# Kernel tuning notes

Measured on AMD Instinct MI355X. Metric: run time of the kernel, lower is better.

Reference implementation:

```python
import jax, jax.numpy as jnp
import numpy as np

N = 100000          # nodes
E = 300000          # edges
F_IN = 128          # num_features
H = 256             # hidden_size
C = 1               # num_classes
G = 2048            # number of graphs in batch
EPS = 1e-5


def setup_inputs() -> dict:
    key = jax.random.key(0)
    ks = jax.random.split(key, 16)
    x = jax.random.normal(ks[0], (N, F_IN), dtype=jnp.float32)
    edge_index = jax.random.randint(ks[1], (2, E), 0, N, dtype=jnp.int64)
    batch = jnp.sort(jax.random.randint(ks[2], (N,), 0, G, dtype=jnp.int64))

    def glorot(k, shape):
        lim = np.sqrt(6.0 / (shape[0] + shape[1]))
        return jax.random.uniform(k, shape, jnp.float32, -lim, lim)

    return {
        "x": x, "edge_index": edge_index, "batch": batch,
        "W1": glorot(ks[3], (F_IN, H)), "b1": jnp.zeros((H,), jnp.float32),
        "W2": glorot(ks[4], (H, H)),    "b2": jnp.zeros((H,), jnp.float32),
        "W3": glorot(ks[5], (H, H)),    "b3": jnp.zeros((H,), jnp.float32),
        "g1": jnp.ones((H,), jnp.float32),  "be1": jnp.zeros((H,), jnp.float32),
        "g2": jnp.ones((H,), jnp.float32),  "be2": jnp.zeros((H,), jnp.float32),
        "g3": jnp.ones((H,), jnp.float32),  "be3": jnp.zeros((H,), jnp.float32),
        "LW1": glorot(ks[6], (H, H)),   "Lb1": jnp.zeros((H,), jnp.float32),
        "LW2": glorot(ks[7], (H, C)),   "Lb2": jnp.zeros((C,), jnp.float32),
    }


def _gcn_conv(x, W, b, src, dst, dinv):
    xw = x @ W                                       # [N, H]
    coeff = (dinv[src] * dinv[dst])[:, None]          # [E, 1]
    msg = xw[src] * coeff                             # gather + scale, [E, H]
    agg = jax.ops.segment_sum(msg, dst, num_segments=x.shape[0])  # scatter-add
    agg = agg + xw * (dinv * dinv)[:, None]           # self-loop term
    return agg + b


def _bn_relu(h, g, be):
    # BatchNorm1d in training mode: batch stats over nodes (biased variance)
    m = h.mean(axis=0)
    v = h.var(axis=0)
    return jax.nn.relu((h - m) * jax.lax.rsqrt(v + EPS) * g + be)


def reference(x, edge_index, batch, W1, b1, W2, b2, W3, b3,
              g1, be1, g2, be2, g3, be3, LW1, Lb1, LW2, Lb2):
    src = edge_index[0]
    dst = edge_index[1]
    # degree with self-loops (computed at destination, as in PyG)
    deg = jax.ops.segment_sum(jnp.ones((E,), jnp.float32), dst, num_segments=N) + 1.0
    dinv = jax.lax.rsqrt(deg)

    h = _bn_relu(_gcn_conv(x, W1, b1, src, dst, dinv), g1, be1)
    h = _bn_relu(_gcn_conv(h, W2, b2, src, dst, dinv), g2, be2)
    h = _bn_relu(_gcn_conv(h, W3, b3, src, dst, dinv), g3, be3)

    # global_add_pool: sum node features per graph
    pooled = jax.ops.segment_sum(h, batch, num_segments=G)   # [G, H]

    out = jax.nn.relu(pooled @ LW1 + Lb1)
    out = out @ LW2 + Lb2                                    # [G, 1]
    return jnp.squeeze(out, axis=1)                          # [G]
```

## Files before the change

### kernel.cpp

```cpp
#include <hip/hip_runtime.h>


typedef __attribute__((ext_vector_type(8))) short bf16x8;
typedef __attribute__((ext_vector_type(4))) float f32x4;

__device__ inline float bf2f(unsigned short u) {
    union { unsigned int i; float f; } v; v.i = ((unsigned int)u) << 16; return v.f;
}
__device__ inline unsigned short f2bf(float f) {
    unsigned int x = __float_as_uint(f);
    unsigned int r = (x + 0x7FFFu + ((x >> 16) & 1u)) >> 16;
    return (unsigned short)r;
}

__device__ inline float4 ld4u(const unsigned short* p) {
    ushort4 u = *(const ushort4*)p;
    return make_float4(bf2f(u.x), bf2f(u.y), bf2f(u.z), bf2f(u.w));
}
__device__ inline void st4u(unsigned short* p, float4 v) {
    ushort4 u; u.x = f2bf(v.x); u.y = f2bf(v.y); u.z = f2bf(v.z); u.w = f2bf(v.w);
    *(ushort4*)p = u;
}

__global__ void count_deg_i(const int* __restrict__ dst, int* __restrict__ deg, int E) {
    int i = blockIdx.x * blockDim.x + threadIdx.x;
    int stride = gridDim.x * blockDim.x;
    for (; i < E; i += stride) atomicAdd(&deg[dst[i]], 1);
}

__global__ __launch_bounds__(256) void scan_partial(
    const int* __restrict__ deg, int* __restrict__ psum, int N)
{
    __shared__ int red[256];
    const int t = threadIdx.x;
    const int i0 = blockIdx.x * 512 + t * 2;
    int s = 0;
    if (i0 < N) s += deg[i0];
    if (i0 + 1 < N) s += deg[i0 + 1];
    red[t] = s;
    __syncthreads();
    for (int off = 128; off > 0; off >>= 1) {
        if (t < off) red[t] += red[t + off];
        __syncthreads();
    }
    if (t == 0) psum[blockIdx.x] = red[0];
}

__global__ __launch_bounds__(1024) void scan_offsets(
    const int* __restrict__ psum, int* __restrict__ poff, int NB,
    int* __restrict__ rowptr, int N)
{
    __shared__ int s[1024];
    const int t = threadIdx.x;
    int v = (t < NB) ? psum[t] : 0;
    s[t] = v;
    __syncthreads();
    for (int off = 1; off < 1024; off <<= 1) {
        int u = (t >= off) ? s[t - off] : 0;
        __syncthreads();
        s[t] += u;
        __syncthreads();
    }
    if (t < NB) poff[t] = s[t] - v;
    if (t == 1023) rowptr[N] = s[1023];
}

__global__ __launch_bounds__(256) void write_rowptr(
    const int* __restrict__ deg, const int* __restrict__ poff,
    int* __restrict__ rowptr, int N)
{
    __shared__ int s[256];
    const int t = threadIdx.x;
    const int i0 = blockIdx.x * 512 + t * 2;
    int e0 = (i0 < N) ? deg[i0] : 0;
    int e1 = (i0 + 1 < N) ? deg[i0 + 1] : 0;
    int sum = e0 + e1;
    s[t] = sum;
    __syncthreads();
    for (int off = 1; off < 256; off <<= 1) {
        int u = (t >= off) ? s[t - off] : 0;
        __syncthreads();
        s[t] += u;
        __syncthreads();
    }
    int excl = s[t] - sum + poff[blockIdx.x];
    if (i0 < N) rowptr[i0] = excl;
    if (i0 + 1 < N) rowptr[i0 + 1] = excl + e0;
}

__global__ void dinv_from_rowptr(const int* __restrict__ rowptr, float* __restrict__ dinv, int N) {
    int i = blockIdx.x * blockDim.x + threadIdx.x;
    if (i < N) dinv[i] = rsqrtf((float)(rowptr[i + 1] - rowptr[i]) + 1.0f);
}

__global__ void fill_csr(const int* __restrict__ src, const int* __restrict__ dst,
                         const int* __restrict__ rowptr, int* __restrict__ cnt,
                         int* __restrict__ col, int E)
{
    int i = blockIdx.x * blockDim.x + threadIdx.x;
    int stride = gridDim.x * blockDim.x;
    for (; i < E; i += stride) {
        int d = dst[i];
        int pos = atomicAdd(&cnt[d], 1);
        col[rowptr[d] + pos] = src[i];
    }
}

__global__ void conv_bf16(const float* __restrict__ in, unsigned short* __restrict__ out,
                          size_t n4)
{
    size_t i = blockIdx.x * (size_t)blockDim.x + threadIdx.x;
    size_t stride = (size_t)gridDim.x * blockDim.x;
    const float4* in4 = (const float4*)in;
    for (; i < n4; i += stride) {
        float4 v = in4[i];
        st4u(out + i * 4, v);
    }
}

__global__ void make_wt(const float* __restrict__ W, unsigned short* __restrict__ WT, int K) {
    int i = blockIdx.x * blockDim.x + threadIdx.x;
    if (i < K * 256) {
        int k = i >> 8, n = i & 255;
        WT[n * K + k] = f2bf(W[i]);
    }
}

__global__ __launch_bounds__(256) void gemm_mfma(
    const unsigned short* __restrict__ A,
    const unsigned short* __restrict__ WT,
    const float* __restrict__ dinv,
    unsigned short* __restrict__ C,
    int K)
{
    __shared__ unsigned short As[128 * 32];
    __shared__ unsigned short Bs[128 * 32];

    const int tid = threadIdx.x;
    const int bm = blockIdx.x * 128;
    const int bn = blockIdx.y * 128;
    const int lane = tid & 63;
    const int wid = tid >> 6;
    const int wr = wid >> 1;
    const int wc = wid & 1;

    const int r0 = tid >> 2;
    const int cc0 = tid & 3;

    f32x4 acc[4][4];
    #pragma unroll
    for (int m = 0; m < 4; ++m)
        #pragma unroll
        for (int n = 0; n < 4; ++n)
            acc[m][n] = (f32x4){0.f, 0.f, 0.f, 0.f};

    uint4* AsV = (uint4*)As;
    uint4* BsV = (uint4*)Bs;

    for (int k0 = 0; k0 < K; k0 += 32) {
        if (k0) __syncthreads();
        {
            const int gcc = (cc0 ^ (r0 & 3)) * 8;
            uint4 va0 = *(const uint4*)(A  + (size_t)(bm + r0)      * K + k0 + gcc);
            uint4 vb0 = *(const uint4*)(WT + (size_t)(bn + r0)      * K + k0 + gcc);
            uint4 va1 = *(const uint4*)(A  + (size_t)(bm + r0 + 64) * K + k0 + gcc);
            uint4 vb1 = *(const uint4*)(WT + (size_t)(bn + r0 + 64) * K + k0 + gcc);
            AsV[r0 * 4 + cc0]        = va0;
            AsV[(r0 + 64) * 4 + cc0] = va1;
            BsV[r0 * 4 + cc0]        = vb0;
            BsV[(r0 + 64) * 4 + cc0] = vb1;
        }
        __syncthreads();

        bf16x8 af[4], bfv[4];
        #pragma unroll
        for (int n = 0; n < 4; ++n) {
            int R = wc * 64 + n * 16 + (lane & 15);
            int pc = (lane >> 4) ^ (R & 3);
            af[n] = *(const bf16x8*)&Bs[R * 32 + pc * 8];
        }
        #pragma unroll
        for (int m = 0; m < 4; ++m) {
            int R = wr * 64 + m * 16 + (lane & 15);
            int pc = (lane >> 4) ^ (R & 3);
            bfv[m] = *(const bf16x8*)&As[R * 32 + pc * 8];
        }
        #pragma unroll
        for (int m = 0; m < 4; ++m)
            #pragma unroll
            for (int n = 0; n < 4; ++n)
                acc[m][n] = __builtin_amdgcn_mfma_f32_16x16x32_bf16(
                    af[n], bfv[m], acc[m][n], 0, 0, 0);
    }

    #pragma unroll
    for (int m = 0; m < 4; ++m) {
        int row = bm + wr * 64 + m * 16 + (lane & 15);
        float di = dinv[row];
        #pragma unroll
        for (int n = 0; n < 4; ++n) {
            int cb = bn + wc * 64 + n * 16 + ((lane >> 4) << 2);
            ushort4 u;
            u.x = f2bf(acc[m][n][0] * di);
            u.y = f2bf(acc[m][n][1] * di);
            u.z = f2bf(acc[m][n][2] * di);
            u.w = f2bf(acc[m][n][3] * di);
            *(ushort4*)(C + (size_t)row * 256 + cb) = u;
        }
    }
}

__global__ __launch_bounds__(256) void gather_bn(
    const unsigned short* __restrict__ xs, const int* __restrict__ rowptr,
    const int* __restrict__ col, const float* __restrict__ dinv,
    const float* __restrict__ b, unsigned short* __restrict__ t_out,
    float* __restrict__ stats, int N)
{
    __shared__ float lred[4][512];
    const int lane = threadIdx.x & 63;
    const int wid = threadIdx.x >> 6;
    const int c4 = lane * 4;
    const float4 bv = *(const float4*)(b + c4);

    float s0 = 0, s1 = 0, s2 = 0, s3 = 0;
    float q0 = 0, q1 = 0, q2 = 0, q3 = 0;

    int w = (blockIdx.x * blockDim.x + threadIdx.x) >> 6;
    const int nw = (gridDim.x * blockDim.x) >> 6;
    for (int n = w; n < N; n += nw) {
        const int e0 = rowptr[n], e1 = rowptr[n + 1];
        float4 acc = ld4u(xs + (size_t)n * 256 + c4);
        for (int e = e0; e < e1; ++e) {
            int s = col[e];
            float4 v = ld4u(xs + (size_t)s * 256 + c4);
            acc.x += v.x; acc.y += v.y; acc.z += v.z; acc.w += v.w;
        }
        const float di = dinv[n];
        float4 t;
        t.x = fmaf(di, acc.x, bv.x);
        t.y = fmaf(di, acc.y, bv.y);
        t.z = fmaf(di, acc.z, bv.z);
        t.w = fmaf(di, acc.w, bv.w);
        st4u(t_out + (size_t)n * 256 + c4, t);
        s0 += t.x; s1 += t.y; s2 += t.z; s3 += t.w;
        q0 += t.x * t.x; q1 += t.y * t.y; q2 += t.z * t.z; q3 += t.w * t.w;
    }
    lred[wid][c4 + 0] = s0; lred[wid][c4 + 1] = s1;
    lred[wid][c4 + 2] = s2; lred[wid][c4 + 3] = s3;
    lred[wid][256 + c4 + 0] = q0; lred[wid][256 + c4 + 1] = q1;
    lred[wid][256 + c4 + 2] = q2; lred[wid][256 + c4 + 3] = q3;
    __syncthreads();
    for (int i = threadIdx.x; i < 512; i += 256) {
        float v = lred[0][i] + lred[1][i] + lred[2][i] + lred[3][i];
        atomicAdd(&stats[i], v);
    }
}

__global__ void bn_finalize(const float* __restrict__ stats,
                            const float* __restrict__ g, const float* __restrict__ be,
                            float* __restrict__ ss, int N)
{
    int f = threadIdx.x;
    float m = stats[f] / (float)N;
    float v = stats[256 + f] / (float)N - m * m;
    float sc = g[f] * rsqrtf(v + 1e-5f);
    ss[f] = sc;
    ss[256 + f] = be[f] - m * sc;
}

__global__ __launch_bounds__(256) void bn_apply(
    const unsigned short* __restrict__ t, const float* __restrict__ ss,
    unsigned short* __restrict__ out, int N)
{
    const float4* sc4 = (const float4*)ss;
    const float4* sh4 = (const float4*)(ss + 256);
    size_t total = (size_t)N * 64;
    size_t stride = (size_t)gridDim.x * blockDim.x;
    for (size_t i = blockIdx.x * (size_t)blockDim.x + threadIdx.x; i < total; i += stride) {
        int c = (int)(i & 63);
        float4 a = ld4u(t + i * 4);
        float4 s = sc4[c], h = sh4[c];
        float4 r;
        r.x = fmaxf(fmaf(a.x, s.x, h.x), 0.f);
        r.y = fmaxf(fmaf(a.y, s.y, h.y), 0.f);
        r.z = fmaxf(fmaf(a.z, s.z, h.z), 0.f);
        r.w = fmaxf(fmaf(a.w, s.w, h.w), 0.f);
        st4u(out + i * 4, r);
    }
}

__global__ __launch_bounds__(256) void pool_seg(
    const unsigned short* __restrict__ t, const int* __restrict__ batch,
    const float* __restrict__ ss, float* __restrict__ pooled, int N)
{
    __shared__ float lred[4][256];
    const int g = blockIdx.x;
    const int lane = threadIdx.x & 63;
    const int wid = threadIdx.x >> 6;
    const int c4 = lane * 4;

    int lo = 0, hi = N;
    while (lo < hi) { int m = (lo + hi) >> 1; if (batch[m] < g) lo = m + 1; else hi = m; }
    const int start = lo;
    hi = N;
    while (lo < hi) { int m = (lo + hi) >> 1; if (batch[m] < g + 1) lo = m + 1; else hi = m; }
    const int end = lo;

    const float4 sc = *(const float4*)(ss + c4);
    const float4 sh = *(const float4*)(ss + 256 + c4);
    float4 acc = make_float4(0.f, 0.f, 0.f, 0.f);
    for (int r = start + wid; r < end; r += 4) {
        float4 a = ld4u(t + (size_t)r * 256 + c4);
        acc.x += fmaxf(fmaf(a.x, sc.x, sh.x), 0.f);
        acc.y += fmaxf(fmaf(a.y, sc.y, sh.y), 0.f);
        acc.z += fmaxf(fmaf(a.z, sc.z, sh.z), 0.f);
        acc.w += fmaxf(fmaf(a.w, sc.w, sh.w), 0.f);
    }
    lred[wid][c4 + 0] = acc.x; lred[wid][c4 + 1] = acc.y;
    lred[wid][c4 + 2] = acc.z; lred[wid][c4 + 3] = acc.w;
    __syncthreads();
    int i = threadIdx.x;
    pooled[(size_t)g * 256 + i] = lred[0][i] + lred[1][i] + lred[2][i] + lred[3][i];
}

__global__ __launch_bounds__(256) void mlp_fused(
    const float* __restrict__ pooled,
    const float* __restrict__ LW1, const float* __restrict__ Lb1,
    const float* __restrict__ LW2, const float* __restrict__ Lb2,
    float* __restrict__ out)
{
    __shared__ float sp[256];
    __shared__ float red[256];
    const int g = blockIdx.x;
    const int t = threadIdx.x;
    sp[t] = pooled[(size_t)g * 256 + t];
    __syncthreads();
    float acc = Lb1[t];
    #pragma unroll 8
    for (int k = 0; k < 256; ++k) acc = fmaf(sp[k], LW1[k * 256 + t], acc);
    acc = fmaxf(acc, 0.f);
    red[t] = acc * LW2[t];
    __syncthreads();
    for (int s = 128; s > 0; s >>= 1) {
        if (t < s) red[t] += red[t + s];
        __syncthreads();
    }
    if (t == 0) out[g] = red[0] + Lb2[0];
}

extern "C" void kernel_launch(void* const* d_in, const int* in_sizes, int n_in,
                              void* d_out, int out_size, void* d_ws, size_t ws_size,
                              hipStream_t stream)
{
    const float* x    = (const float*)d_in[0];
    const int*   ei   = (const int*)d_in[1];
    const int*   batch= (const int*)d_in[2];
    const float* W1 = (const float*)d_in[3];  const float* b1 = (const float*)d_in[4];
    const float* W2 = (const float*)d_in[5];  const float* b2 = (const float*)d_in[6];
    const float* W3 = (const float*)d_in[7];  const float* b3 = (const float*)d_in[8];
    const float* g1 = (const float*)d_in[9];  const float* be1= (const float*)d_in[10];
    const float* g2 = (const float*)d_in[11]; const float* be2= (const float*)d_in[12];
    const float* g3 = (const float*)d_in[13]; const float* be3= (const float*)d_in[14];
    const float* LW1= (const float*)d_in[15]; const float* Lb1= (const float*)d_in[16];
    const float* LW2= (const float*)d_in[17]; const float* Lb2= (const float*)d_in[18];

    const int N = in_sizes[2];
    const int E = in_sizes[1] / 2;
    const int F = in_sizes[0] / N;
    const int H = in_sizes[4];
    const int G = out_size;
    const int Mp = (N + 127) & ~127;
    const int NB = (N + 511) / 512;
    const int* src = ei;
    const int* dst = ei + E;
    const size_t NHp = (size_t)Mp * H;

    const float* Wl[3] = {W1, W2, W3};
    const float* bl[3] = {b1, b2, b3};
    const float* gl[3] = {g1, g2, g3};
    const float* bel[3]= {be1, be2, be3};

    char* p = (char*)d_ws;
    unsigned short* TB = (unsigned short*)p;  p += NHp * 2;
    unsigned short* XS = (unsigned short*)p;  p += NHp * 2;
    unsigned short* HB = (unsigned short*)p;  p += NHp * 2;
    unsigned short* XB = HB;
    float* dinv = (float*)p;           p += (((size_t)Mp * 4) + 255) & ~(size_t)255;
    int* degi  = (int*)p;              p += (((size_t)N * 4) + 255) & ~(size_t)255;
    float* stats = (float*)p;          p += 2048;
    float* ss    = (float*)p;          p += 2048;
    int* psum   = (int*)p;             p += 4096;
    int* poff   = (int*)p;             p += 4096;
    float* pooled= (float*)p;          p += (size_t)G * H * 4;
    int* rowptr = (int*)p;             p += (((size_t)(N + 1) * 4) + 255) & ~(size_t)255;
    int* col    = (int*)p;             p += (((size_t)E * 4) + 255) & ~(size_t)255;
    unsigned short* WTb = (unsigned short*)p;  p += (size_t)H * H * 2;

    hipMemsetAsync(degi, 0, (size_t)N * sizeof(int), stream);
    count_deg_i<<<1024, 256, 0, stream>>>(dst, degi, E);
    scan_partial<<<NB, 256, 0, stream>>>(degi, psum, N);
    scan_offsets<<<1, 1024, 0, stream>>>(psum, poff, NB, rowptr, N);
    write_rowptr<<<NB, 256, 0, stream>>>(degi, poff, rowptr, N);
    dinv_from_rowptr<<<(N + 255) / 256, 256, 0, stream>>>(rowptr, dinv, N);
    hipMemsetAsync(degi, 0, (size_t)N * sizeof(int), stream);
    fill_csr<<<1024, 256, 0, stream>>>(src, dst, rowptr, degi, col, E);

    conv_bf16<<<2048, 256, 0, stream>>>(x, XB, (size_t)N * F / 4);

    for (int L = 0; L < 3; ++L) {
        const int K = (L == 0) ? F : H;
        make_wt<<<(K * 256 + 255) / 256, 256, 0, stream>>>(Wl[L], WTb, K);
        dim3 grid(Mp / 128, H / 128);
        gemm_mfma<<<grid, 256, 0, stream>>>((L == 0) ? XB : HB, WTb, dinv, XS, K);
        hipMemsetAsync(stats, 0, 512 * sizeof(float), stream);
        gather_bn<<<1024, 256, 0, stream>>>(XS, rowptr, col, dinv, bl[L], TB, stats, N);
        bn_finalize<<<1, 256, 0, stream>>>(stats, gl[L], bel[L], ss, N);
        if (L < 2)
            bn_apply<<<2048, 256, 0, stream>>>(TB, ss, HB, N);
        else
            pool_seg<<<G, 256, 0, stream>>>(TB, batch, ss, pooled, N);
    }

    mlp_fused<<<G, 256, 0, stream>>>(pooled, LW1, Lb1, LW2, Lb2, (float*)d_out);
}
```

Before: 623.0 us.

## Fuse BN+ReLU into GEMM A-load and interleave four nodes in gather

Removes the standalone bn_apply kernel by applying the batch-norm scale/shift and ReLU to the A tile as it is loaded in the next layer's GEMM, reading the pre-BN buffer directly. This drops one full read and write of the N×256 bf16 activation per layer. The gather kernel now handles four nodes per wave iteration, interleaving their edge loops to keep more independent loads in flight. The cost is extra ALU work in the GEMM load path and more registers and divergent predication in the gather loop.

New measurement: 594.0 us. 1.05x faster.

```diff
diff --git a/kernel.cpp b/kernel.cpp
--- a/kernel.cpp
+++ b/kernel.cpp
@@ -14,7 +14,7 @@
 }
 
 __device__ inline float4 ld4u(const unsigned short* p) {
-    ushort4 u = *(const ushort4*)p;
+    ushort4 u = *(const ushort4*)(p);
     return make_float4(bf2f(u.x), bf2f(u.y), bf2f(u.z), bf2f(u.w));
 }
 __device__ inline void st4u(unsigned short* p, float4 v) {
@@ -126,10 +126,32 @@
     }
 }
 
+__device__ inline unsigned int bn2(unsigned int w, float sL, float hL, float sH, float hH) {
+    float lo = bf2f((unsigned short)(w & 0xFFFFu));
+    float hi = bf2f((unsigned short)(w >> 16));
+    lo = fmaxf(fmaf(lo, sL, hL), 0.f);
+    hi = fmaxf(fmaf(hi, sH, hH), 0.f);
+    return (unsigned int)f2bf(lo) | ((unsigned int)f2bf(hi) << 16);
+}
+__device__ inline uint4 bn8(uint4 v, const float* __restrict__ ss, int c) {
+    float4 sA = *(const float4*)(ss + c);
+    float4 sB = *(const float4*)(ss + c + 4);
+    float4 hA = *(const float4*)(ss + 256 + c);
+    float4 hB = *(const float4*)(ss + 256 + c + 4);
+    uint4 r;
+    r.x = bn2(v.x, sA.x, hA.x, sA.y, hA.y);
+    r.y = bn2(v.y, sA.z, hA.z, sA.w, hA.w);
+    r.z = bn2(v.z, sB.x, hB.x, sB.y, hB.y);
+    r.w = bn2(v.w, sB.z, hB.z, sB.w, hB.w);
+    return r;
+}
+
+template<int FUSE_BN>
 __global__ __launch_bounds__(256) void gemm_mfma(
     const unsigned short* __restrict__ A,
     const unsigned short* __restrict__ WT,
     const float* __restrict__ dinv,
+    const float* __restrict__ ss,
     unsigned short* __restrict__ C,
     int K)
 {
@@ -165,6 +187,10 @@
             uint4 vb0 = *(const uint4*)(WT + (size_t)(bn + r0)      * K + k0 + gcc);
             uint4 va1 = *(const uint4*)(A  + (size_t)(bm + r0 + 64) * K + k0 + gcc);
             uint4 vb1 = *(const uint4*)(WT + (size_t)(bn + r0 + 64) * K + k0 + gcc);
+            if (FUSE_BN) {
+                va0 = bn8(va0, ss, k0 + gcc);
+                va1 = bn8(va1, ss, k0 + gcc);
+            }
             AsV[r0 * 4 + cc0]        = va0;
             AsV[(r0 + 64) * 4 + cc0] = va1;
             BsV[r0 * 4 + cc0]        = vb0;
@@ -225,26 +251,83 @@
     float s0 = 0, s1 = 0, s2 = 0, s3 = 0;
     float q0 = 0, q1 = 0, q2 = 0, q3 = 0;
 
-    int w = (blockIdx.x * blockDim.x + threadIdx.x) >> 6;
+    const int w = (blockIdx.x * blockDim.x + threadIdx.x) >> 6;
     const int nw = (gridDim.x * blockDim.x) >> 6;
-    for (int n = w; n < N; n += nw) {
-        const int e0 = rowptr[n], e1 = rowptr[n + 1];
-        float4 acc = ld4u(xs + (size_t)n * 256 + c4);
-        for (int e = e0; e < e1; ++e) {
-            int s = col[e];
-            float4 v = ld4u(xs + (size_t)s * 256 + c4);
-            acc.x += v.x; acc.y += v.y; acc.z += v.z; acc.w += v.w;
-        }
-        const float di = dinv[n];
-        float4 t;
-        t.x = fmaf(di, acc.x, bv.x);
-        t.y = fmaf(di, acc.y, bv.y);
-        t.z = fmaf(di, acc.z, bv.z);
-        t.w = fmaf(di, acc.w, bv.w);
-        st4u(t_out + (size_t)n * 256 + c4, t);
-        s0 += t.x; s1 += t.y; s2 += t.z; s3 += t.w;
-        q0 += t.x * t.x; q1 += t.y * t.y; q2 += t.z * t.z; q3 += t.w * t.w;
-    }
+
+    for (int n0 = w; n0 < N; n0 += nw * 4) {
+        const int nA = n0;
+        const int nB = n0 + nw;
+        const int nC = n0 + 2 * nw;
+        const int nD = n0 + 3 * nw;
+        const bool hB = nB < N, hC = nC < N, hD = nD < N;
+
+        int eA = rowptr[nA], eA1 = rowptr[nA + 1];
+        int eB = 0, eB1 = 0, eC = 0, eC1 = 0, eD = 0, eD1 = 0;
+        if (hB) { eB = rowptr[nB]; eB1 = rowptr[nB + 1]; }
+        if (hC) { eC = rowptr[nC]; eC1 = rowptr[nC + 1]; }
+        if (hD) { eD = rowptr[nD]; eD1 = rowptr[nD + 1]; }
+
+        float4 aA = ld4u(xs + (size_t)nA * 256 + c4);
+        float4 aB = make_float4(0.f, 0.f, 0.f, 0.f), aC = aB, aD = aB;
+        if (hB) aB = ld4u(xs + (size_t)nB * 256 + c4);
+        if (hC) aC = ld4u(xs + (size_t)nC * 256 + c4);
+        if (hD) aD = ld4u(xs + (size_t)nD * 256 + c4);
+
+        while ((eA < eA1) | (eB < eB1) | (eC < eC1) | (eD < eD1)) {
+            int sA = -1, sB = -1, sC = -1, sD = -1;
+            if (eA < eA1) sA = col[eA++];
+            if (eB < eB1) sB = col[eB++];
+            if (eC < eC1) sC = col[eC++];
+            if (eD < eD1) sD = col[eD++];
+            float4 vA, vB, vC, vD;
+            if (sA >= 0) vA = ld4u(xs + (size_t)sA * 256 + c4);
+            if (sB >= 0) vB = ld4u(xs + (size_t)sB * 256 + c4);
+            if (sC >= 0) vC = ld4u(xs + (size_t)sC * 256 + c4);
+            if (sD >= 0) vD = ld4u(xs + (size_t)sD * 256 + c4);
+            if (sA >= 0) { aA.x += vA.x; aA.y += vA.y; aA.z += vA.z; aA.w += vA.w; }
+            if (sB >= 0) { aB.x += vB.x; aB.y += vB.y; aB.z += vB.z; aB.w += vB.w; }
+            if (sC >= 0) { aC.x += vC.x; aC.y += vC.y; aC.z += vC.z; aC.w += vC.w; }
+            if (sD >= 0) { aD.x += vD.x; aD.y += vD.y; aD.z += vD.z; aD.w += vD.w; }
+        }
+
+        {
+            float di = dinv[nA];
+            float4 t;
+            t.x = fmaf(di, aA.x, bv.x); t.y = fmaf(di, aA.y, bv.y);
+            t.z = fmaf(di, aA.z, bv.z); t.w = fmaf(di, aA.w, bv.w);
+            st4u(t_out + (size_t)nA * 256 + c4, t);
+            s0 += t.x; s1 += t.y; s2 += t.z; s3 += t.w;
+            q0 += t.x * t.x; q1 += t.y * t.y; q2 += t.z * t.z; q3 += t.w * t.w;
+        }
+        if (hB) {
+            float di = dinv[nB];
+            float4 t;
+            t.x = fmaf(di, aB.x, bv.x); t.y = fmaf(di, aB.y, bv.y);
+            t.z = fmaf(di, aB.z, bv.z); t.w = fmaf(di, aB.w, bv.w);
+            st4u(t_out + (size_t)nB * 256 + c4, t);
+            s0 += t.x; s1 += t.y; s2 += t.z; s3 += t.w;
+            q0 += t.x * t.x; q1 += t.y * t.y; q2 += t.z * t.z; q3 += t.w * t.w;
+        }
+        if (hC) {
+            float di = dinv[nC];
+            float4 t;
+            t.x = fmaf(di, aC.x, bv.x); t.y = fmaf(di, aC.y, bv.y);
+            t.z = fmaf(di, aC.z, bv.z); t.w = fmaf(di, aC.w, bv.w);
+            st4u(t_out + (size_t)nC * 256 + c4, t);
+            s0 += t.x; s1 += t.y; s2 += t.z; s3 += t.w;
+            q0 += t.x * t.x; q1 += t.y * t.y; q2 += t.z * t.z; q3 += t.w * t.w;
+        }
+        if (hD) {
+            float di = dinv[nD];
+            float4 t;
+            t.x = fmaf(di, aD.x, bv.x); t.y = fmaf(di, aD.y, bv.y);
+            t.z = fmaf(di, aD.z, bv.z); t.w = fmaf(di, aD.w, bv.w);
+            st4u(t_out + (size_t)nD * 256 + c4, t);
+            s0 += t.x; s1 += t.y; s2 += t.z; s3 += t.w;
+            q0 += t.x * t.x; q1 += t.y * t.y; q2 += t.z * t.z; q3 += t.w * t.w;
+        }
+    }
+
     lred[wid][c4 + 0] = s0; lred[wid][c4 + 1] = s1;
     lred[wid][c4 + 2] = s2; lred[wid][c4 + 3] = s3;
     lred[wid][256 + c4 + 0] = q0; lred[wid][256 + c4 + 1] = q1;
@@ -266,27 +349,6 @@
     float sc = g[f] * rsqrtf(v + 1e-5f);
     ss[f] = sc;
     ss[256 + f] = be[f] - m * sc;
-}
-
-__global__ __launch_bounds__(256) void bn_apply(
-    const unsigned short* __restrict__ t, const float* __restrict__ ss,
-    unsigned short* __restrict__ out, int N)
-{
-    const float4* sc4 = (const float4*)ss;
-    const float4* sh4 = (const float4*)(ss + 256);
-    size_t total = (size_t)N * 64;
-    size_t stride = (size_t)gridDim.x * blockDim.x;
-    for (size_t i = blockIdx.x * (size_t)blockDim.x + threadIdx.x; i < total; i += stride) {
-        int c = (int)(i & 63);
-        float4 a = ld4u(t + i * 4);
-        float4 s = sc4[c], h = sh4[c];
-        float4 r;
-        r.x = fmaxf(fmaf(a.x, s.x, h.x), 0.f);
-        r.y = fmaxf(fmaf(a.y, s.y, h.y), 0.f);
-        r.z = fmaxf(fmaf(a.z, s.z, h.z), 0.f);
-        r.w = fmaxf(fmaf(a.w, s.w, h.w), 0.f);
-        st4u(out + i * 4, r);
-    }
 }
 
 __global__ __launch_bounds__(256) void pool_seg(
@@ -383,8 +445,7 @@
     char* p = (char*)d_ws;
     unsigned short* TB = (unsigned short*)p;  p += NHp * 2;
     unsigned short* XS = (unsigned short*)p;  p += NHp * 2;
-    unsigned short* HB = (unsigned short*)p;  p += NHp * 2;
-    unsigned short* XB = HB;
+    unsigned short* XB = (unsigned short*)p;  p += (size_t)Mp * 128 * 2;
     float* dinv = (float*)p;           p += (((size_t)Mp * 4) + 255) & ~(size_t)255;
     int* degi  = (int*)p;              p += (((size_t)N * 4) + 255) & ~(size_t)255;
     float* stats = (float*)p;          p += 2048;
@@ -411,15 +472,15 @@
         const int K = (L == 0) ? F : H;
         make_wt<<<(K * 256 + 255) / 256, 256, 0, stream>>>(Wl[L], WTb, K);
         dim3 grid(Mp / 128, H / 128);
-        gemm_mfma<<<grid, 256, 0, stream>>>((L == 0) ? XB : HB, WTb, dinv, XS, K);
+        if (L == 0)
+            gemm_mfma<0><<<grid, 256, 0, stream>>>(XB, WTb, dinv, nullptr, XS, K);
+        else
+            gemm_mfma<1><<<grid, 256, 0, stream>>>(TB, WTb, dinv, ss, XS, K);
         hipMemsetAsync(stats, 0, 512 * sizeof(float), stream);
         gather_bn<<<1024, 256, 0, stream>>>(XS, rowptr, col, dinv, bl[L], TB, stats, N);
         bn_finalize<<<1, 256, 0, stream>>>(stats, gl[L], bel[L], ss, N);
-        if (L < 2)
-            bn_apply<<<2048, 256, 0, stream>>>(TB, ss, HB, N);
-        else
-            pool_seg<<<G, 256, 0, stream>>>(TB, batch, ss, pooled, N);
-    }
-
+    }
+
+    pool_seg<<<G, 256, 0, stream>>>(TB, batch, ss, pooled, N);
     mlp_fused<<<G, 256, 0, stream>>>(pooled, LW1, Lb1, LW2, Lb2, (float*)d_out);
 }
```
